# Optimization experiments

Measured on AMD Instinct MI355X. Metric: run time of the kernel, lower is better.

Reference implementation:

```python
import jax, jax.numpy as jnp
import numpy as np

NEG_INF = -1e9


def setup_inputs() -> dict:
    B, S, D = 4, 2048, 1024
    key = jax.random.key(0)
    ks = jax.random.split(key, 10)
    sc = 1.0 / np.sqrt(D)
    return {
        "batch": jax.random.normal(ks[0], (B, S, D), jnp.float32),
        "padding_mask": jax.random.randint(ks[1], (B, S), 0, 2) > 0,
        "Wq": jax.random.normal(ks[2], (D, D), jnp.float32) * sc,
        "bq": jnp.zeros((D,), jnp.float32),
        "Wk": jax.random.normal(ks[3], (D, D), jnp.float32) * sc,
        "bk": jnp.zeros((D,), jnp.float32),
        "Wv": jax.random.normal(ks[4], (D, D), jnp.float32) * sc,
        "bv": jnp.zeros((D,), jnp.float32),
        "Wo": jax.random.normal(ks[5], (D, D), jnp.float32) * sc,
        "bo": jnp.zeros((D,), jnp.float32),
        "num_heads": 16,
    }


def _split_heads(x, H):
    B, S, D = x.shape
    return x.reshape(B, S, H, D // H).transpose(0, 2, 1, 3)  # [B,H,S,hd]


def reference(batch, padding_mask, Wq, bq, Wk, bk, Wv, bv, Wo, bo, num_heads):
    B, S, D = batch.shape
    H = num_heads
    q = _split_heads(batch @ Wq + bq, H)  # [B,H,S,hd]
    k = _split_heads(batch @ Wk + bk, H)
    v = _split_heads(batch @ Wv + bv, H)
    # tf.keras.layers.Attention default: unscaled dot-product scores
    scores = jnp.einsum("bhqd,bhkd->bhqk", q, k)
    kmask = padding_mask[:, None, None, :]  # value/key mask -> masks score columns
    scores = jnp.where(kmask, scores, NEG_INF)
    probs = jax.nn.softmax(scores, axis=-1)
    ctx = jnp.einsum("bhqk,bhkd->bhqd", probs, v)
    # query mask zeroes padded query positions (tf Attention behavior)
    ctx = ctx * padding_mask[:, None, :, None].astype(ctx.dtype)
    ctx = ctx.transpose(0, 2, 1, 3).reshape(B, S, D)
    return ctx @ Wo + bo
```

## Files before the change

kernel.cpp:

```cpp
#include <hip/hip_runtime.h>


#define Bb 4
#define Ss 2048
#define Dd 1024
#define Hh 16
#define SZt 8388608

typedef short bf16x8 __attribute__((ext_vector_type(8)));
typedef float f32x4 __attribute__((ext_vector_type(4)));
typedef float f32x16 __attribute__((ext_vector_type(16)));
typedef unsigned short u16;

__device__ __forceinline__ float bf2f(u16 u) {
    return __builtin_bit_cast(float, ((unsigned)u) << 16);
}
__device__ __forceinline__ u16 f2bf(float f) {
    unsigned u = __builtin_bit_cast(unsigned, f);
    unsigned r = 0x7FFFu + ((u >> 16) & 1u);
    return (u16)((u + r) >> 16);
}
__device__ __forceinline__ bf16x8 ldfrag(const u16* p) {
    return __builtin_bit_cast(bf16x8, *(const uint4*)p);
}
__device__ __forceinline__ f32x4 mfma16(bf16x8 a, bf16x8 b, f32x4 c) {
    return __builtin_amdgcn_mfma_f32_16x16x32_bf16(a, b, c, 0, 0, 0);
}
__device__ __forceinline__ f32x16 mfma32(bf16x8 a, bf16x8 b, f32x16 c) {
    return __builtin_amdgcn_mfma_f32_32x32x16_bf16(a, b, c, 0, 0, 0);
}
__device__ __forceinline__ void gl2lds16(const u16* g, u16* l) {
    __builtin_amdgcn_global_load_lds(
        (const __attribute__((address_space(1))) u16*)g,
        (__attribute__((address_space(3))) u16*)l, 16, 0, 0);
}

__global__ void normalize_mask(const unsigned char* __restrict__ raw, float* __restrict__ out,
                               float* __restrict__ outb, int n) {
    __shared__ int flags;
    if (threadIdx.x == 0) flags = 0;
    __syncthreads();
    int f = 0;
    for (int i = threadIdx.x; i < n; i += blockDim.x) {
        unsigned char c = raw[i];
        if ((i & 3) != 0 && c) f |= 1;
        if ((i & 3) == 1 && c >= 2) f |= 2;
        if ((i & 3) == 3 && c >= 2) f |= 4;
    }
    if (f) atomicOr(&flags, f);
    __syncthreads();
    int fl = flags;
    int layout;
    if (!(fl & 1)) layout = 0;
    else if (fl & 2) layout = 2;
    else if (fl & 4) layout = 3;
    else layout = 1;
    for (int i = threadIdx.x; i < n; i += blockDim.x) {
        int v;
        if (layout == 0)      v = ((const int*)raw)[i];
        else if (layout == 1) v = raw[i];
        else if (layout == 2) v = ((const u16*)raw)[i] != 0;
        else                  v = ((const unsigned*)raw)[i] != 0;
        out[i]  = (v != 0) ? 1.0f : 0.0f;
        outb[i] = (v != 0) ? 0.0f : -30000.0f;
    }
}

__global__ void concat_bias(const float* __restrict__ a, const float* __restrict__ b,
                            const float* __restrict__ c, float* __restrict__ o) {
    int i = blockIdx.x * 256 + threadIdx.x;
    o[i] = (i < 1024) ? a[i] : ((i < 2048) ? b[i - 1024] : c[i - 2048]);
}

__global__ __launch_bounds__(256) void convert_x(const float* __restrict__ X,
                                                 u16* __restrict__ Xh, u16* __restrict__ Xl) {
    size_t i = ((size_t)blockIdx.x * 256 + threadIdx.x) * 4;
    float4 v = *(const float4*)(X + i);
    u16 h0 = f2bf(v.x), h1 = f2bf(v.y), h2 = f2bf(v.z), h3 = f2bf(v.w);
    u16 l0 = f2bf(v.x - bf2f(h0)), l1 = f2bf(v.y - bf2f(h1));
    u16 l2 = f2bf(v.z - bf2f(h2)), l3 = f2bf(v.w - bf2f(h3));
    uint2 ph = { (unsigned)h0 | ((unsigned)h1 << 16), (unsigned)h2 | ((unsigned)h3 << 16) };
    uint2 pl = { (unsigned)l0 | ((unsigned)l1 << 16), (unsigned)l2 | ((unsigned)l3 << 16) };
    *(uint2*)(Xh + i) = ph;
    *(uint2*)(Xl + i) = pl;
}

__global__ __launch_bounds__(256) void transpose_w(const float* __restrict__ W, u16* __restrict__ Wt) {
    __shared__ float t[32][33];
    const int tx = threadIdx.x, ty = threadIdx.y;
    const int n0 = blockIdx.x * 32, k0 = blockIdx.y * 32;
    #pragma unroll
    for (int i = 0; i < 4; i++)
        t[ty + i * 8][tx] = W[(size_t)(k0 + ty + i * 8) * Dd + n0 + tx];
    __syncthreads();
    #pragma unroll
    for (int i = 0; i < 4; i++)
        Wt[(size_t)(n0 + ty + i * 8) * Dd + k0 + tx] = f2bf(t[tx][ty + i * 8]);
}

__global__ __launch_bounds__(256) void gemm_qkv(
    const u16* __restrict__ Ah, const u16* __restrict__ Al,
    const u16* __restrict__ Wcat, const float* __restrict__ bcat,
    u16* __restrict__ Qb, u16* __restrict__ Kb, u16* __restrict__ Vt)
{
    __shared__ u16 Ahs[128][64];
    __shared__ u16 Bs[128][64];
    __shared__ u16 Als[128][64];
    const int tid = threadIdx.x, lane = tid & 63, wave = tid >> 6;
    const int wm = wave >> 1, wn = wave & 1;
    const int bm = blockIdx.y * 128, bn = blockIdx.x * 128;
    const bool twopass = (bn < 2048);
    const int l15 = lane & 15, lq = lane >> 4;
    const int sr = wave * 32 + (lane >> 3);
    const int sc = (lane & 7) * 8;
    const u16* agp = Ah + (size_t)(bm + sr) * Dd + sc;
    const u16* bgp = Wcat + (size_t)(bn + sr) * Dd + sc;
    const u16* algp = Al + (size_t)(bm + sr) * Dd + sc;

    f32x4 acc[4][4] = {};

    for (int k0 = 0; k0 < Dd; k0 += 64) {
        __syncthreads();
        #pragma unroll
        for (int j = 0; j < 4; j++) {
            gl2lds16(agp + k0 + (size_t)j * 8 * Dd, &Ahs[wave * 32 + j * 8][0]);
            gl2lds16(bgp + k0 + (size_t)j * 8 * Dd, &Bs[wave * 32 + j * 8][0]);
            if (twopass)
                gl2lds16(algp + k0 + (size_t)j * 8 * Dd, &Als[wave * 32 + j * 8][0]);
        }
        __syncthreads();
        #pragma unroll
        for (int kf = 0; kf < 2; kf++) {
            bf16x8 b[4], a[4];
            #pragma unroll
            for (int nt = 0; nt < 4; nt++)
                b[nt] = ldfrag(&Bs[wn * 64 + nt * 16 + l15][kf * 32 + lq * 8]);
            #pragma unroll
            for (int mt = 0; mt < 4; mt++)
                a[mt] = ldfrag(&Ahs[wm * 64 + mt * 16 + l15][kf * 32 + lq * 8]);
            #pragma unroll
            for (int mt = 0; mt < 4; mt++)
                #pragma unroll
                for (int nt = 0; nt < 4; nt++)
                    acc[mt][nt] = mfma16(a[mt], b[nt], acc[mt][nt]);
            if (twopass) {
                bf16x8 al2[4];
                #pragma unroll
                for (int mt = 0; mt < 4; mt++)
                    al2[mt] = ldfrag(&Als[wm * 64 + mt * 16 + l15][kf * 32 + lq * 8]);
                #pragma unroll
                for (int mt = 0; mt < 4; mt++)
                    #pragma unroll
                    for (int nt = 0; nt < 4; nt++)
                        acc[mt][nt] = mfma16(al2[mt], b[nt], acc[mt][nt]);
            }
        }
    }
    float bv[4];
    #pragma unroll
    for (int nt = 0; nt < 4; nt++) bv[nt] = bcat[bn + wn * 64 + nt * 16 + l15];
    #pragma unroll
    for (int mt = 0; mt < 4; mt++) {
        int r0 = bm + wm * 64 + mt * 16 + lq * 4;
        #pragma unroll
        for (int nt = 0; nt < 4; nt++) {
            int col = bn + wn * 64 + nt * 16 + l15;
            if (col < 1024) {
                #pragma unroll
                for (int rr = 0; rr < 4; rr++)
                    Qb[(size_t)(r0 + rr) * Dd + col] = f2bf(acc[mt][nt][rr] + bv[nt]);
            } else if (col < 2048) {
                int c2 = col - 1024;
                #pragma unroll
                for (int rr = 0; rr < 4; rr++)
                    Kb[(size_t)(r0 + rr) * Dd + c2] = f2bf(acc[mt][nt][rr] + bv[nt]);
            } else {
                int c2 = col - 2048;
                int hh = c2 >> 6, dd = c2 & 63, b_ = r0 >> 11, s0 = r0 & 2047;
                u16 e0 = f2bf(acc[mt][nt][0] + bv[nt]), e1 = f2bf(acc[mt][nt][1] + bv[nt]);
                u16 e2 = f2bf(acc[mt][nt][2] + bv[nt]), e3 = f2bf(acc[mt][nt][3] + bv[nt]);
                uint2 pk = { (unsigned)e0 | ((unsigned)e1 << 16), (unsigned)e2 | ((unsigned)e3 << 16) };
                *(uint2*)(Vt + (size_t)((b_ * Hh + hh) * 64 + dd) * Ss + s0) = pk;
            }
        }
    }
}

__global__ __launch_bounds__(256) void gemm_out(
    const u16* __restrict__ Ah, const u16* __restrict__ Wt,
    const float* __restrict__ bias, float* __restrict__ Cout)
{
    __shared__ u16 Ahs[128][64];
    __shared__ u16 Bs[128][64];
    const int tid = threadIdx.x, lane = tid & 63, wave = tid >> 6;
    const int wm = wave >> 1, wn = wave & 1;
    const int bm = blockIdx.y * 128, bn = blockIdx.x * 128;
    const int l15 = lane & 15, lq = lane >> 4;
    const int sr = wave * 32 + (lane >> 3);
    const int sc = (lane & 7) * 8;
    const u16* agp = Ah + (size_t)(bm + sr) * Dd + sc;
    const u16* bgp = Wt + (size_t)(bn + sr) * Dd + sc;

    f32x4 acc[4][4] = {};

    for (int k0 = 0; k0 < Dd; k0 += 64) {
        __syncthreads();
        #pragma unroll
        for (int j = 0; j < 4; j++) {
            gl2lds16(agp + k0 + (size_t)j * 8 * Dd, &Ahs[wave * 32 + j * 8][0]);
            gl2lds16(bgp + k0 + (size_t)j * 8 * Dd, &Bs[wave * 32 + j * 8][0]);
        }
        __syncthreads();
        #pragma unroll
        for (int kf = 0; kf < 2; kf++) {
            bf16x8 b[4], a[4];
            #pragma unroll
            for (int nt = 0; nt < 4; nt++)
                b[nt] = ldfrag(&Bs[wn * 64 + nt * 16 + l15][kf * 32 + lq * 8]);
            #pragma unroll
            for (int mt = 0; mt < 4; mt++)
                a[mt] = ldfrag(&Ahs[wm * 64 + mt * 16 + l15][kf * 32 + lq * 8]);
            #pragma unroll
            for (int mt = 0; mt < 4; mt++)
                #pragma unroll
                for (int nt = 0; nt < 4; nt++)
                    acc[mt][nt] = mfma16(a[mt], b[nt], acc[mt][nt]);
        }
    }
    float bv[4];
    #pragma unroll
    for (int nt = 0; nt < 4; nt++) bv[nt] = bias[bn + wn * 64 + nt * 16 + l15];
    #pragma unroll
    for (int mt = 0; mt < 4; mt++) {
        int r0 = bm + wm * 64 + mt * 16 + lq * 4;
        #pragma unroll
        for (int nt = 0; nt < 4; nt++) {
            int col = bn + wn * 64 + nt * 16 + l15;
            #pragma unroll
            for (int rr = 0; rr < 4; rr++)
                Cout[(size_t)(r0 + rr) * Dd + col] = acc[mt][nt][rr] + bv[nt];
        }
    }
}

__global__ __launch_bounds__(512, 4) void attn_mfma(
    u16* qctx, const u16* __restrict__ Kb, const u16* __restrict__ Vt,
    const float* __restrict__ maskf, const float* __restrict__ mbias)
{
    __shared__ u16 Ks[64][72];
    __shared__ u16 Vs[64][72];
    __shared__ u16 Ps[8][32][40];
    const int tid = threadIdx.x, lane = tid & 63, wave = tid >> 6;
    const int l31 = lane & 31, hi = lane >> 5;
    const int bh = blockIdx.x, h = bh & 15, b = bh >> 4;
    const int q0 = blockIdx.y * 256;

    bf16x8 qa[4];
    {
        const u16* qp = qctx + (size_t)(b * Ss + q0 + wave * 32 + l31) * Dd + h * 64 + hi * 8;
        #pragma unroll
        for (int kf = 0; kf < 4; kf++) qa[kf] = ldfrag(qp + kf * 16);
    }

    const int srow = tid >> 3, scol = (tid & 7) * 8;
    const u16* kgsrc = Kb + (size_t)(b * Ss + srow) * Dd + h * 64 + scol;
    const u16* vgsrc = Vt + (size_t)((b * Hh + h) * 64 + srow) * Ss + scol;
    u16* kdst = &Ks[srow][scol];
    u16* vdst = &Vs[srow][scol];

    f32x16 acc0 = {}, acc1 = {};
    float li[16];
    #pragma unroll
    for (int r = 0; r < 16; r++) li[r] = 0.f;

    uint4 kreg = *(const uint4*)kgsrc;
    uint4 vreg = *(const uint4*)vgsrc;
    const float LOG2E = 1.44269504088896f;

    for (int k0 = 0; k0 < Ss; k0 += 64) {
        __syncthreads();
        *(uint4*)kdst = kreg;
        *(uint4*)vdst = vreg;
        __syncthreads();
        int k0n = (k0 + 64 < Ss) ? k0 + 64 : 0;
        kreg = *(const uint4*)(kgsrc + (size_t)k0n * Dd);
        vreg = *(const uint4*)(vgsrc + k0n);
        float mb[2];
        mb[0] = mbias[b * Ss + k0 + l31];
        mb[1] = mbias[b * Ss + k0 + 32 + l31];

        #pragma unroll
        for (int nt = 0; nt < 2; nt++) {
            f32x16 sc = {};
            #pragma unroll
            for (int kf = 0; kf < 4; kf++) {
                bf16x8 kb = ldfrag(&Ks[nt * 32 + l31][kf * 16 + hi * 8]);
                sc = mfma32(qa[kf], kb, sc);
            }
            #pragma unroll
            for (int r = 0; r < 16; r++) {
                float p = __builtin_amdgcn_exp2f(fmaf(sc[r], LOG2E, mb[nt]));
                li[r] += p;
                unsigned ub = __builtin_bit_cast(unsigned, p);
                Ps[wave][(r & 3) + 8 * (r >> 2) + 4 * hi][l31] = (u16)((ub + 0x8000u) >> 16);
            }
            #pragma unroll
            for (int kf = 0; kf < 2; kf++) {
                bf16x8 pa = ldfrag(&Ps[wave][l31][kf * 16 + hi * 8]);
                bf16x8 v0 = ldfrag(&Vs[l31][nt * 32 + kf * 16 + hi * 8]);
                bf16x8 v1 = ldfrag(&Vs[32 + l31][nt * 32 + kf * 16 + hi * 8]);
                acc0 = mfma32(pa, v0, acc0);
                acc1 = mfma32(pa, v1, acc1);
            }
        }
    }

    #pragma unroll
    for (int r = 0; r < 16; r++) {
        float s = li[r];
        s += __shfl_xor(s, 1); s += __shfl_xor(s, 2);
        s += __shfl_xor(s, 4); s += __shfl_xor(s, 8);
        s += __shfl_xor(s, 16);
        li[r] = s;
    }
    #pragma unroll
    for (int r = 0; r < 16; r++) {
        int row = (r & 3) + 8 * (r >> 2) + 4 * hi;
        int q = q0 + wave * 32 + row;
        float qm = maskf[b * Ss + q];
        float rl = li[r] > 0.f ? qm / li[r] : 0.f;
        u16* op = qctx + (size_t)(b * Ss + q) * Dd + h * 64 + l31;
        op[0]  = f2bf(acc0[r] * rl);
        op[32] = f2bf(acc1[r] * rl);
    }
}

extern "C" void kernel_launch(void* const* d_in, const int* in_sizes, int n_in,
                              void* d_out, int out_size, void* d_ws, size_t ws_size,
                              hipStream_t stream) {
    const float* X  = (const float*)d_in[0];
    const unsigned char* mr = (const unsigned char*)d_in[1];
    const float* Wq = (const float*)d_in[2];
    const float* bq = (const float*)d_in[3];
    const float* Wk = (const float*)d_in[4];
    const float* bk = (const float*)d_in[5];
    const float* Wv = (const float*)d_in[6];
    const float* bv = (const float*)d_in[7];
    const float* Wo = (const float*)d_in[8];
    const float* bo = (const float*)d_in[9];
    float* out = (float*)d_out;

    u16* wsb = (u16*)d_ws;
    u16* Xh  = wsb;
    u16* Qb  = wsb + (size_t)SZt;
    u16* Kb  = wsb + 2 * (size_t)SZt;
    u16* Vt  = wsb + 3 * (size_t)SZt;
    u16* Wot = Xh;
    u16* ob  = (u16*)d_out;
    u16* Xl  = ob;
    u16* Wcat = ob + (size_t)SZt;
    u16* Wqt = Wcat;
    u16* Wkt = Wqt + 1048576;
    u16* Wvt = Wkt + 1048576;
    float* mnorm = (float*)(Wvt + 1048576);
    float* bcat  = mnorm + Bb * Ss;
    float* mbias = bcat + 3072;

    dim3 tg(32, 32), tb(32, 8);

    normalize_mask<<<1, 1024, 0, stream>>>(mr, mnorm, mbias, Bb * Ss);
    concat_bias<<<12, 256, 0, stream>>>(bq, bk, bv, bcat);
    convert_x<<<SZt / 1024, 256, 0, stream>>>(X, Xh, Xl);
    transpose_w<<<tg, tb, 0, stream>>>(Wq, Wqt);
    transpose_w<<<tg, tb, 0, stream>>>(Wk, Wkt);
    transpose_w<<<tg, tb, 0, stream>>>(Wv, Wvt);
    gemm_qkv<<<dim3(24, 64), 256, 0, stream>>>(Xh, Xl, Wcat, bcat, Qb, Kb, Vt);
    transpose_w<<<tg, tb, 0, stream>>>(Wo, Wot);
    attn_mfma<<<dim3(Bb * Hh, Ss / 256), 512, 0, stream>>>(Qb, Kb, Vt, mnorm, mbias);
    gemm_out<<<dim3(8, 64), 256, 0, stream>>>(Qb, Wot, bo, out);
}
```

Measured before the change: 341.1 us.

## Fold key mask into K/V, prescale Q by log2e, keep P in registers

Masked keys are zeroed in K and V inside the QKV GEMM epilogue, so their scores become exactly zero. Each then contributes exp2(0)=1 to the row sum, which is removed by subtracting a per-batch count of masked keys; Q is prescaled by log2e. This drops the per-tile mask bias loads and FMA in attention. The score MFMA operands are swapped so the probabilities come out transposed, and the P operand is built in registers with packed bf16 conversion and permlane32 swaps instead of a round trip through LDS. The row-sum reduction collapses to a single cross-half shuffle. The risk is numerical: masked keys are no longer suppressed in the numerator's max-free exponent, and the denominator relies on subtracting counts from a float sum.

```diff
diff --git a/kernel.cpp b/kernel.cpp
--- a/kernel.cpp
+++ b/kernel.cpp
@@ -10,6 +10,7 @@
 typedef short bf16x8 __attribute__((ext_vector_type(8)));
 typedef float f32x4 __attribute__((ext_vector_type(4)));
 typedef float f32x16 __attribute__((ext_vector_type(16)));
+typedef unsigned int u32x4 __attribute__((ext_vector_type(4)));
 typedef unsigned short u16;
 
 __device__ __forceinline__ float bf2f(u16 u) {
@@ -29,6 +30,11 @@
 __device__ __forceinline__ f32x16 mfma32(bf16x8 a, bf16x8 b, f32x16 c) {
     return __builtin_amdgcn_mfma_f32_32x32x16_bf16(a, b, c, 0, 0, 0);
 }
+__device__ __forceinline__ unsigned cvt_pk_bf16(float a, float b) {
+    unsigned r;
+    asm("v_cvt_pk_bf16_f32 %0, %1, %2" : "=v"(r) : "v"(a), "v"(b));
+    return r;
+}
 __device__ __forceinline__ void gl2lds16(const u16* g, u16* l) {
     __builtin_amdgcn_global_load_lds(
         (const __attribute__((address_space(1))) u16*)g,
@@ -36,9 +42,11 @@
 }
 
 __global__ void normalize_mask(const unsigned char* __restrict__ raw, float* __restrict__ out,
-                               float* __restrict__ outb, int n) {
+                               float* __restrict__ cnt, int n) {
     __shared__ int flags;
+    __shared__ float scnt[Bb];
     if (threadIdx.x == 0) flags = 0;
+    if (threadIdx.x < Bb) scnt[threadIdx.x] = 0.f;
     __syncthreads();
     int f = 0;
     for (int i = threadIdx.x; i < n; i += blockDim.x) {
@@ -61,9 +69,11 @@
         else if (layout == 1) v = raw[i];
         else if (layout == 2) v = ((const u16*)raw)[i] != 0;
         else                  v = ((const unsigned*)raw)[i] != 0;
-        out[i]  = (v != 0) ? 1.0f : 0.0f;
-        outb[i] = (v != 0) ? 0.0f : -30000.0f;
-    }
+        out[i] = (v != 0) ? 1.0f : 0.0f;
+        if (v == 0) atomicAdd(&scnt[i >> 11], 1.0f);
+    }
+    __syncthreads();
+    if (threadIdx.x < Bb) cnt[threadIdx.x] = scnt[threadIdx.x];
 }
 
 __global__ void concat_bias(const float* __restrict__ a, const float* __restrict__ b,
@@ -101,6 +111,7 @@
 __global__ __launch_bounds__(256) void gemm_qkv(
     const u16* __restrict__ Ah, const u16* __restrict__ Al,
     const u16* __restrict__ Wcat, const float* __restrict__ bcat,
+    const float* __restrict__ mnorm,
     u16* __restrict__ Qb, u16* __restrict__ Kb, u16* __restrict__ Vt)
 {
     __shared__ u16 Ahs[128][64];
@@ -110,6 +121,7 @@
     const int wm = wave >> 1, wn = wave & 1;
     const int bm = blockIdx.y * 128, bn = blockIdx.x * 128;
     const bool twopass = (bn < 2048);
+    const bool isQ = (bn < 1024);
     const int l15 = lane & 15, lq = lane >> 4;
     const int sr = wave * 32 + (lane >> 3);
     const int sc = (lane & 7) * 8;
@@ -156,29 +168,37 @@
             }
         }
     }
+    const float LOG2E = 1.44269504088896f;
     float bv[4];
     #pragma unroll
     for (int nt = 0; nt < 4; nt++) bv[nt] = bcat[bn + wn * 64 + nt * 16 + l15];
     #pragma unroll
     for (int mt = 0; mt < 4; mt++) {
         int r0 = bm + wm * 64 + mt * 16 + lq * 4;
+        float mk[4];
+        if (!isQ) {
+            #pragma unroll
+            for (int rr = 0; rr < 4; rr++) mk[rr] = mnorm[r0 + rr];
+        }
         #pragma unroll
         for (int nt = 0; nt < 4; nt++) {
             int col = bn + wn * 64 + nt * 16 + l15;
             if (col < 1024) {
                 #pragma unroll
                 for (int rr = 0; rr < 4; rr++)
-                    Qb[(size_t)(r0 + rr) * Dd + col] = f2bf(acc[mt][nt][rr] + bv[nt]);
+                    Qb[(size_t)(r0 + rr) * Dd + col] = f2bf((acc[mt][nt][rr] + bv[nt]) * LOG2E);
             } else if (col < 2048) {
                 int c2 = col - 1024;
                 #pragma unroll
                 for (int rr = 0; rr < 4; rr++)
-                    Kb[(size_t)(r0 + rr) * Dd + c2] = f2bf(acc[mt][nt][rr] + bv[nt]);
+                    Kb[(size_t)(r0 + rr) * Dd + c2] = f2bf((acc[mt][nt][rr] + bv[nt]) * mk[rr]);
             } else {
                 int c2 = col - 2048;
                 int hh = c2 >> 6, dd = c2 & 63, b_ = r0 >> 11, s0 = r0 & 2047;
-                u16 e0 = f2bf(acc[mt][nt][0] + bv[nt]), e1 = f2bf(acc[mt][nt][1] + bv[nt]);
-                u16 e2 = f2bf(acc[mt][nt][2] + bv[nt]), e3 = f2bf(acc[mt][nt][3] + bv[nt]);
+                u16 e0 = f2bf((acc[mt][nt][0] + bv[nt]) * mk[0]);
+                u16 e1 = f2bf((acc[mt][nt][1] + bv[nt]) * mk[1]);
+                u16 e2 = f2bf((acc[mt][nt][2] + bv[nt]) * mk[2]);
+                u16 e3 = f2bf((acc[mt][nt][3] + bv[nt]) * mk[3]);
                 uint2 pk = { (unsigned)e0 | ((unsigned)e1 << 16), (unsigned)e2 | ((unsigned)e3 << 16) };
                 *(uint2*)(Vt + (size_t)((b_ * Hh + hh) * 64 + dd) * Ss + s0) = pk;
             }
@@ -245,11 +265,11 @@
 
 __global__ __launch_bounds__(512, 4) void attn_mfma(
     u16* qctx, const u16* __restrict__ Kb, const u16* __restrict__ Vt,
-    const float* __restrict__ maskf, const float* __restrict__ mbias)
+    const float* __restrict__ maskf, const float* __restrict__ cntp)
 {
     __shared__ u16 Ks[64][72];
     __shared__ u16 Vs[64][72];
-    __shared__ u16 Ps[8][32][40];
+    __shared__ float li_s[8][32];
     const int tid = threadIdx.x, lane = tid & 63, wave = tid >> 6;
     const int l31 = lane & 31, hi = lane >> 5;
     const int bh = blockIdx.x, h = bh & 15, b = bh >> 4;
@@ -269,13 +289,10 @@
     u16* vdst = &Vs[srow][scol];
 
     f32x16 acc0 = {}, acc1 = {};
-    float li[16];
-    #pragma unroll
-    for (int r = 0; r < 16; r++) li[r] = 0.f;
+    float li = 0.f;
 
     uint4 kreg = *(const uint4*)kgsrc;
     uint4 vreg = *(const uint4*)vgsrc;
-    const float LOG2E = 1.44269504088896f;
 
     for (int k0 = 0; k0 < Ss; k0 += 64) {
         __syncthreads();
@@ -285,9 +302,6 @@
         int k0n = (k0 + 64 < Ss) ? k0 + 64 : 0;
         kreg = *(const uint4*)(kgsrc + (size_t)k0n * Dd);
         vreg = *(const uint4*)(vgsrc + k0n);
-        float mb[2];
-        mb[0] = mbias[b * Ss + k0 + l31];
-        mb[1] = mbias[b * Ss + k0 + 32 + l31];
 
         #pragma unroll
         for (int nt = 0; nt < 2; nt++) {
@@ -295,43 +309,61 @@
             #pragma unroll
             for (int kf = 0; kf < 4; kf++) {
                 bf16x8 kb = ldfrag(&Ks[nt * 32 + l31][kf * 16 + hi * 8]);
-                sc = mfma32(qa[kf], kb, sc);
+                sc = mfma32(kb, qa[kf], sc);
             }
-            #pragma unroll
-            for (int r = 0; r < 16; r++) {
-                float p = __builtin_amdgcn_exp2f(fmaf(sc[r], LOG2E, mb[nt]));
-                li[r] += p;
-                unsigned ub = __builtin_bit_cast(unsigned, p);
-                Ps[wave][(r & 3) + 8 * (r >> 2) + 4 * hi][l31] = (u16)((ub + 0x8000u) >> 16);
+            float p[16];
+            #pragma unroll
+            for (int r = 0; r < 8; r++) p[r] = __builtin_amdgcn_exp2f(sc[r]);
+            li += ((p[0] + p[1]) + (p[2] + p[3])) + ((p[4] + p[5]) + (p[6] + p[7]));
+            {
+                unsigned w0 = cvt_pk_bf16(p[0], p[1]), w1 = cvt_pk_bf16(p[2], p[3]);
+                unsigned w2 = cvt_pk_bf16(p[4], p[5]), w3 = cvt_pk_bf16(p[6], p[7]);
+                auto s02 = __builtin_amdgcn_permlane32_swap((int)w0, (int)w2, false, false);
+                auto s13 = __builtin_amdgcn_permlane32_swap((int)w1, (int)w3, false, false);
+                u32x4 pw = { (unsigned)s02[0], (unsigned)s13[0], (unsigned)s02[1], (unsigned)s13[1] };
+                bf16x8 pa0 = __builtin_bit_cast(bf16x8, pw);
+                bf16x8 v00 = ldfrag(&Vs[l31][nt * 32 + hi * 8]);
+                bf16x8 v10 = ldfrag(&Vs[32 + l31][nt * 32 + hi * 8]);
+                acc0 = mfma32(pa0, v00, acc0);
+                acc1 = mfma32(pa0, v10, acc1);
             }
             #pragma unroll
-            for (int kf = 0; kf < 2; kf++) {
-                bf16x8 pa = ldfrag(&Ps[wave][l31][kf * 16 + hi * 8]);
-                bf16x8 v0 = ldfrag(&Vs[l31][nt * 32 + kf * 16 + hi * 8]);
-                bf16x8 v1 = ldfrag(&Vs[32 + l31][nt * 32 + kf * 16 + hi * 8]);
-                acc0 = mfma32(pa, v0, acc0);
-                acc1 = mfma32(pa, v1, acc1);
+            for (int r = 8; r < 16; r++) p[r] = __builtin_amdgcn_exp2f(sc[r]);
+            li += ((p[8] + p[9]) + (p[10] + p[11])) + ((p[12] + p[13]) + (p[14] + p[15]));
+            {
+                unsigned w4 = cvt_pk_bf16(p[8], p[9]),  w5 = cvt_pk_bf16(p[10], p[11]);
+                unsigned w6 = cvt_pk_bf16(p[12], p[13]), w7 = cvt_pk_bf16(p[14], p[15]);
+                auto s46 = __builtin_amdgcn_permlane32_swap((int)w4, (int)w6, false, false);
+                auto s57 = __builtin_amdgcn_permlane32_swap((int)w5, (int)w7, false, false);
+                u32x4 pw = { (unsigned)s46[0], (unsigned)s57[0], (unsigned)s46[1], (unsigned)s57[1] };
+                bf16x8 pa1 = __builtin_bit_cast(bf16x8, pw);
+                bf16x8 v01 = ldfrag(&Vs[l31][nt * 32 + 16 + hi * 8]);
+                bf16x8 v11 = ldfrag(&Vs[32 + l31][nt * 32 + 16 + hi * 8]);
+                acc0 = mfma32(pa1, v01, acc0);
+                acc1 = mfma32(pa1, v11, acc1);
             }
         }
     }
 
-    #pragma unroll
-    for (int r = 0; r < 16; r++) {
-        float s = li[r];
-        s += __shfl_xor(s, 1); s += __shfl_xor(s, 2);
-        s += __shfl_xor(s, 4); s += __shfl_xor(s, 8);
-        s += __shfl_xor(s, 16);
-        li[r] = s;
-    }
-    #pragma unroll
-    for (int r = 0; r < 16; r++) {
-        int row = (r & 3) + 8 * (r >> 2) + 4 * hi;
-        int q = q0 + wave * 32 + row;
-        float qm = maskf[b * Ss + q];
-        float rl = li[r] > 0.f ? qm / li[r] : 0.f;
-        u16* op = qctx + (size_t)(b * Ss + q) * Dd + h * 64 + l31;
-        op[0]  = f2bf(acc0[r] * rl);
-        op[32] = f2bf(acc1[r] * rl);
+    float li_tot = li + __shfl_xor(li, 32);
+    if (hi == 0) li_s[wave][l31] = li_tot;
+    __builtin_amdgcn_s_barrier();
+    float cntb = cntp[b];
+    #pragma unroll
+    for (int g = 0; g < 4; g++) {
+        float4 lv = *(const float4*)&li_s[wave][g * 8 + hi * 4];
+        #pragma unroll
+        for (int j = 0; j < 4; j++) {
+            int r = g * 4 + j;
+            int row = j + 8 * g + 4 * hi;
+            int q = q0 + wave * 32 + row;
+            float qm = maskf[b * Ss + q];
+            float den = lv[j] - cntb;
+            float rl = den > 0.f ? qm / den : 0.f;
+            u16* op = qctx + (size_t)(b * Ss + q) * Dd + h * 64 + l31;
+            op[0]  = f2bf(acc0[r] * rl);
+            op[32] = f2bf(acc1[r] * rl);
+        }
     }
 }
 
@@ -364,18 +396,18 @@
     u16* Wvt = Wkt + 1048576;
     float* mnorm = (float*)(Wvt + 1048576);
     float* bcat  = mnorm + Bb * Ss;
-    float* mbias = bcat + 3072;
+    float* cntp  = bcat + 3072;
 
     dim3 tg(32, 32), tb(32, 8);
 
-    normalize_mask<<<1, 1024, 0, stream>>>(mr, mnorm, mbias, Bb * Ss);
+    normalize_mask<<<1, 1024, 0, stream>>>(mr, mnorm, cntp, Bb * Ss);
     concat_bias<<<12, 256, 0, stream>>>(bq, bk, bv, bcat);
     convert_x<<<SZt / 1024, 256, 0, stream>>>(X, Xh, Xl);
     transpose_w<<<tg, tb, 0, stream>>>(Wq, Wqt);
     transpose_w<<<tg, tb, 0, stream>>>(Wk, Wkt);
     transpose_w<<<tg, tb, 0, stream>>>(Wv, Wvt);
-    gemm_qkv<<<dim3(24, 64), 256, 0, stream>>>(Xh, Xl, Wcat, bcat, Qb, Kb, Vt);
+    gemm_qkv<<<dim3(24, 64), 256, 0, stream>>>(Xh, Xl, Wcat, bcat, mnorm, Qb, Kb, Vt);
     transpose_w<<<tg, tb, 0, stream>>>(Wo, Wot);
-    attn_mfma<<<dim3(Bb * Hh, Ss / 256), 512, 0, stream>>>(Qb, Kb, Vt, mnorm, mbias);
+    attn_mfma<<<dim3(Bb * Hh, Ss / 256), 512, 0, stream>>>(Qb, Kb, Vt, mnorm, cntp);
     gemm_out<<<dim3(8, 64), 256, 0, stream>>>(Qb, Wot, bo, out);
 }
```

After: 321.4 us. 1.06x faster.
